# Performance work log

Measured on AMD Instinct MI355X. Metric: run time of the kernel, lower is better.

## Reference

```python
import jax, jax.numpy as jnp
import numpy as np

N_FILT = 80
FILT_DIM = 251
FS = 16000.0
MIN_FREQ = 50.0


def _kernel_gauss(amp, f1, f2, t):
    # Gaussian-windowed (Gabor-like) bandpass impulse response: band edges f1<f2 (Hz)
    fc = 0.5 * (f1 + f2)
    bw = f2 - f1
    return amp * jnp.exp(-2.0 * (jnp.pi * bw) ** 2 * t ** 2) * jnp.cos(2.0 * jnp.pi * fc * t)


def _norm_pm1(ir):
    # per-filter: scale to [-1,1] then zero-mean, matching the torch code
    mn = jnp.min(ir, axis=-1, keepdims=True)
    mx = jnp.max(ir, axis=-1, keepdims=True)
    ir = 2.0 * (ir - mn) / (mx - mn + 1e-6) - 1.0
    return ir - jnp.mean(ir, axis=-1, keepdims=True)


def _build_filters(norm_f1, norm_f2, norm_f3, norm_f4, amp1, amp2):
    N = FILT_DIM
    t = (jnp.arange(1, N + 1, dtype=jnp.float32) / FS)  # linspace(1,N,N)/fs
    mf = MIN_FREQ / FS
    f1 = jnp.clip(jnp.abs(norm_f1) + mf, 0.0, 0.5)
    f2 = jnp.clip(f1 + jnp.abs(norm_f2 - f1) + mf, 0.0, 0.5)
    f3 = jnp.clip(jnp.abs(norm_f3) + mf, 0.0, 0.5)
    f4 = jnp.clip(f3 + jnp.abs(norm_f4 - f3) + mf, 0.0, 0.5)
    a1 = jnp.abs(amp1)[:, None]
    a2 = jnp.abs(amp2)[:, None]
    ir1 = _norm_pm1(_kernel_gauss(a1, (f1 * FS)[:, None], (f2 * FS)[:, None], t[None, :]))
    ir2 = _norm_pm1(_kernel_gauss(a2, (f3 * FS)[:, None], (f4 * FS)[:, None], t[None, :]))
    pad = N // 2
    # cross-correlation of ir1 with ir2 (torch conv1d semantics), padding N//2 -> length N (N odd)
    def xcorr(a, b):
        return jnp.correlate(jnp.pad(a, (pad, pad)), b[::-1], mode='valid')[::-1] if False else jnp.convolve(jnp.pad(a, (pad, pad)), b[::-1], mode='valid')
    casc = jax.vmap(xcorr)(ir1, ir2)  # [N_filt, N]
    casc = _norm_pm1(casc)
    n = jnp.linspace(0.0, N, N)
    window = (0.54 - 0.46 * jnp.cos(2.0 * jnp.pi * n / N)).astype(jnp.float32)
    return casc * window[None, :]  # [N_filt, N]


def setup_inputs() -> dict:
    key = jax.random.key(0)
    ks = jax.random.split(key, 5)
    x = jax.random.normal(ks[0], (8, 1, 64000), dtype=jnp.float32)
    norm_f1 = jax.random.uniform(ks[1], (N_FILT,), dtype=jnp.float32) * 0.3
    norm_f2 = norm_f1 + jax.random.uniform(ks[2], (N_FILT,), dtype=jnp.float32) * 0.05
    norm_f3 = jax.random.uniform(ks[3], (N_FILT,), dtype=jnp.float32) * 0.3
    norm_f4 = norm_f3 + jax.random.uniform(ks[4], (N_FILT,), dtype=jnp.float32) * 0.05
    amp1 = jnp.ones((N_FILT,), dtype=jnp.float32)
    amp2 = jnp.ones((N_FILT,), dtype=jnp.float32)
    return {"x": x, "norm_f1": norm_f1, "norm_f2": norm_f2, "norm_f3": norm_f3,
            "norm_f4": norm_f4, "amp1": amp1, "amp2": amp2}


def reference(x, norm_f1, norm_f2, norm_f3, norm_f4, amp1, amp2):
    filters = _build_filters(norm_f1, norm_f2, norm_f3, norm_f4, amp1, amp2)
    w = filters[:, None, :]  # [O=N_filt, I=1, K]
    out = jax.lax.conv_general_dilated(
        x, w, window_strides=(1,), padding='VALID',
        dimension_numbers=('NCH', 'OIH', 'NCH'))
    return out  # [B, N_filt, T-K+1]
```

## Files before the change

kernel.cpp:

```cpp
#include <hip/hip_runtime.h>

#define FDIM   251
#define NFILT  80
#define KPAD   256
#define T_IN   64000
#define T_OUT  63750
#define NCHUNK 512
#define NXB    125
#define NFT    5
#define CPYLEN 392
#define XSTOT  (8 * CPYLEN)

typedef short bf16x8 __attribute__((ext_vector_type(8)));
typedef float f32x4  __attribute__((ext_vector_type(4)));

__device__ __forceinline__ unsigned short f2bf(float f) {
  unsigned int u = __float_as_uint(f);
  unsigned int r = (u + 0x7fffu + ((u >> 16) & 1u)) >> 16;
  return (unsigned short)r;
}
__device__ __forceinline__ unsigned int packbf(float a, float b) {
  return (unsigned int)f2bf(a) | ((unsigned int)f2bf(b) << 16);
}

__device__ __forceinline__ void norm_pm1_shared(float* a, float* scratch, int tid) {
  float v  = (tid < FDIM) ? a[tid] : 0.f;
  float mn = (tid < FDIM) ? v : 1e30f;
  float mx = (tid < FDIM) ? v : -1e30f;
  #pragma unroll
  for (int o = 32; o > 0; o >>= 1) {
    mn = fminf(mn, __shfl_down(mn, o));
    mx = fmaxf(mx, __shfl_down(mx, o));
  }
  const int wid = tid >> 6;
  if ((tid & 63) == 0) { scratch[wid] = mn; scratch[4 + wid] = mx; }
  __syncthreads();
  if (tid == 0) {
    scratch[0] = fminf(fminf(scratch[0], scratch[1]), fminf(scratch[2], scratch[3]));
    scratch[4] = fmaxf(fmaxf(scratch[4], scratch[5]), fmaxf(scratch[6], scratch[7]));
  }
  __syncthreads();
  const float gmn = scratch[0], gmx = scratch[4];
  const float nv = 2.f * (v - gmn) / (gmx - gmn + 1e-6f) - 1.f;
  __syncthreads();
  float s = (tid < FDIM) ? nv : 0.f;
  #pragma unroll
  for (int o = 32; o > 0; o >>= 1) s += __shfl_down(s, o);
  if ((tid & 63) == 0) scratch[wid] = s;
  __syncthreads();
  if (tid == 0) scratch[0] = (scratch[0] + scratch[1] + scratch[2] + scratch[3]) / 251.f;
  __syncthreads();
  const float mean = scratch[0];
  if (tid < FDIM) a[tid] = nv - mean;
  __syncthreads();
}

__global__ __launch_bounds__(256) void build_filters_kernel(
    const float* __restrict__ nf1, const float* __restrict__ nf2,
    const float* __restrict__ nf3, const float* __restrict__ nf4,
    const float* __restrict__ amp1, const float* __restrict__ amp2,
    unsigned short* __restrict__ Wbf) {
  __shared__ float ir1[FDIM], ir2[FDIM], casc[FDIM];
  __shared__ float scratch[8];
  const int f = blockIdx.x, tid = threadIdx.x;
  const float FS  = 16000.f;
  const float MF  = 50.f / 16000.f;
  const float PIF = 3.14159265358979323846f;
  const float TPI = 6.28318530717958647692f;

  const float f1 = fminf(fmaxf(fabsf(nf1[f]) + MF, 0.f), 0.5f);
  const float f2 = fminf(fmaxf(f1 + fabsf(nf2[f] - f1) + MF, 0.f), 0.5f);
  const float f3 = fminf(fmaxf(fabsf(nf3[f]) + MF, 0.f), 0.5f);
  const float f4 = fminf(fmaxf(f3 + fabsf(nf4[f] - f3) + MF, 0.f), 0.5f);
  const float a1 = fabsf(amp1[f]);
  const float a2 = fabsf(amp2[f]);

  if (tid < FDIM) {
    const float t = (float)(tid + 1) / FS;
    {
      const float fcs = 0.5f * (f1 + f2) * FS, bws = (f2 - f1) * FS;
      const float pb = PIF * bws;
      ir1[tid] = a1 * expf(-2.f * pb * pb * (t * t)) * cosf(TPI * fcs * t);
    }
    {
      const float fcs = 0.5f * (f3 + f4) * FS, bws = (f4 - f3) * FS;
      const float pb = PIF * bws;
      ir2[tid] = a2 * expf(-2.f * pb * pb * (t * t)) * cosf(TPI * fcs * t);
    }
  }
  __syncthreads();
  norm_pm1_shared(ir1, scratch, tid);
  norm_pm1_shared(ir2, scratch, tid);

  if (tid < FDIM) {
    const int i = tid;
    const int plo = (i - 125 > 0) ? (i - 125) : 0;
    const int phi = (i + 125 < 250) ? (i + 125) : 250;
    float s = 0.f;
    for (int p = plo; p <= phi; ++p) s += ir1[p] * ir2[p + 125 - i];
    casc[i] = s;
  }
  __syncthreads();
  norm_pm1_shared(casc, scratch, tid);

  if (tid < KPAD) {
    float v = 0.f;
    if (tid < FDIM) {
      const float win = 0.54f - 0.46f * cosf(TPI * ((float)tid / 250.f));
      v = casc[tid] * win;
    }
    Wbf[(size_t)f * KPAD + tid] = f2bf(v);
  }
}

__global__ __launch_bounds__(256, 4) void conv_mfma_kernel(
    const float* __restrict__ xin, const unsigned short* __restrict__ Wbf,
    float* __restrict__ outp) {
  __shared__ __align__(16) unsigned int xs[XSTOT];
  const int tid = threadIdx.x;
  const int n0  = blockIdx.x * NCHUNK;
  const int b   = blockIdx.y;
  const int l   = tid & 63, w = tid >> 6;
  const int m   = l & 15, h = l >> 4;

  const float* xg = xin + (size_t)b * T_IN;
  for (int i = tid; i < CPYLEN - 4; i += 256) {
    float e[10];
    #pragma unroll
    for (int q = 0; q < 10; ++q) {
      const int g = n0 + 2 * i + q;
      e[q] = (g < T_IN) ? xg[g] : 0.f;
    }
    #pragma unroll
    for (int j = 0; j < 8; ++j)
      xs[j * CPYLEN + i] = packbf(e[j], e[j + 1]);
  }
  __syncthreads();

  const unsigned int* psrc = xs + (m & 7) * CPYLEN;
  const int lane_q = h + (m >> 3);
  const int tw0 = w * 128;
  const short* Wp = (const short*)Wbf;

  #pragma unroll 1
  for (int ft = 0; ft < NFT; ++ft) {
    bf16x8 afr[8];
    #pragma unroll
    for (int c = 0; c < 8; ++c)
      afr[c] = *(const bf16x8*)(Wp + (ft * 16 + m) * KPAD + c * 32 + h * 8);

    const size_t rowh = ((size_t)b * NFILT + ft * 16 + 4 * h) * T_OUT;

    for (int jp = 0; jp < 4; ++jp) {
      const int qA = ((tw0 + jp * 32) >> 3) + lane_q;
      f32x4 accA = (f32x4){0.f, 0.f, 0.f, 0.f};
      f32x4 accB = (f32x4){0.f, 0.f, 0.f, 0.f};

      #pragma unroll
      for (int c = 0; c < 8; ++c) {
        const bf16x8 xa = *(const bf16x8*)(psrc + 4 * (qA + 4 * c));
        const bf16x8 xb = *(const bf16x8*)(psrc + 4 * (qA + 2 + 4 * c));
        accA = __builtin_amdgcn_mfma_f32_16x16x32_bf16(afr[c], xa, accA, 0, 0, 0);
        accB = __builtin_amdgcn_mfma_f32_16x16x32_bf16(afr[c], xb, accB, 0, 0, 0);
      }

      const int tgA = n0 + tw0 + jp * 32 + m;
      const int tgB = tgA + 16;
      #pragma unroll
      for (int r = 0; r < 4; ++r) {
        const size_t rb = rowh + (size_t)r * T_OUT;
        if (tgA < T_OUT) outp[rb + tgA] = accA[r];
        if (tgB < T_OUT) outp[rb + tgB] = accB[r];
      }
    }
  }
}

extern "C" void kernel_launch(void* const* d_in, const int* in_sizes, int n_in,
                              void* d_out, int out_size, void* d_ws, size_t ws_size,
                              hipStream_t stream) {
  const float* x    = (const float*)d_in[0];
  const float* nf1  = (const float*)d_in[1];
  const float* nf2  = (const float*)d_in[2];
  const float* nf3  = (const float*)d_in[3];
  const float* nf4  = (const float*)d_in[4];
  const float* amp1 = (const float*)d_in[5];
  const float* amp2 = (const float*)d_in[6];
  unsigned short* Wbf = (unsigned short*)d_ws;
  float* out = (float*)d_out;

  build_filters_kernel<<<NFILT, 256, 0, stream>>>(nf1, nf2, nf3, nf4, amp1, amp2, Wbf);

  dim3 grid(NXB, 8);
  conv_mfma_kernel<<<grid, 256, 0, stream>>>(x, Wbf, out);
}
```

Before: 69.05 us.

## Split conv into MFMA producer waves and store consumer waves via LDS double buffer

Doubles the block to 512 threads. Four waves compute MFMA tiles into a double-buffered LDS output staging area, and four other waves copy the previous filter tile to global memory with coalesced float2 stores. This overlaps compute with output writes and replaces the strided scattered per-lane stores with contiguous row writes. In exchange it uses about 66KB of extra LDS per block, which limits occupancy, and adds a block-wide barrier per stage.

```diff
diff --git a/kernel.cpp b/kernel.cpp
--- a/kernel.cpp
+++ b/kernel.cpp
@@ -10,6 +10,8 @@
 #define NFT    5
 #define CPYLEN 392
 #define XSTOT  (8 * CPYLEN)
+#define BUFSTR 514
+#define BUFSZ  (16 * BUFSTR)
 
 typedef short bf16x8 __attribute__((ext_vector_type(8)));
 typedef float f32x4  __attribute__((ext_vector_type(4)));
@@ -113,18 +115,19 @@
   }
 }
 
-__global__ __launch_bounds__(256, 4) void conv_mfma_kernel(
+__global__ __launch_bounds__(512, 4) void conv_mfma_kernel(
     const float* __restrict__ xin, const unsigned short* __restrict__ Wbf,
     float* __restrict__ outp) {
   __shared__ __align__(16) unsigned int xs[XSTOT];
+  __shared__ __align__(16) float obuf[2 * BUFSZ];
   const int tid = threadIdx.x;
   const int n0  = blockIdx.x * NCHUNK;
   const int b   = blockIdx.y;
-  const int l   = tid & 63, w = tid >> 6;
+  const int l   = tid & 63, wid = tid >> 6;
   const int m   = l & 15, h = l >> 4;
 
   const float* xg = xin + (size_t)b * T_IN;
-  for (int i = tid; i < CPYLEN - 4; i += 256) {
+  for (int i = tid; i < CPYLEN - 4; i += 512) {
     float e[10];
     #pragma unroll
     for (int q = 0; q < 10; ++q) {
@@ -139,40 +142,61 @@
 
   const unsigned int* psrc = xs + (m & 7) * CPYLEN;
   const int lane_q = h + (m >> 3);
+  const short* Wp = (const short*)Wbf;
+  const int w   = wid & 3;
   const int tw0 = w * 128;
-  const short* Wp = (const short*)Wbf;
+  const int wid2 = wid - 4;
 
   #pragma unroll 1
-  for (int ft = 0; ft < NFT; ++ft) {
-    bf16x8 afr[8];
-    #pragma unroll
-    for (int c = 0; c < 8; ++c)
-      afr[c] = *(const bf16x8*)(Wp + (ft * 16 + m) * KPAD + c * 32 + h * 8);
-
-    const size_t rowh = ((size_t)b * NFILT + ft * 16 + 4 * h) * T_OUT;
-
-    for (int jp = 0; jp < 4; ++jp) {
-      const int qA = ((tw0 + jp * 32) >> 3) + lane_q;
-      f32x4 accA = (f32x4){0.f, 0.f, 0.f, 0.f};
-      f32x4 accB = (f32x4){0.f, 0.f, 0.f, 0.f};
-
-      #pragma unroll
-      for (int c = 0; c < 8; ++c) {
-        const bf16x8 xa = *(const bf16x8*)(psrc + 4 * (qA + 4 * c));
-        const bf16x8 xb = *(const bf16x8*)(psrc + 4 * (qA + 2 + 4 * c));
-        accA = __builtin_amdgcn_mfma_f32_16x16x32_bf16(afr[c], xa, accA, 0, 0, 0);
-        accB = __builtin_amdgcn_mfma_f32_16x16x32_bf16(afr[c], xb, accB, 0, 0, 0);
+  for (int p = 0; p < NFT + 1; ++p) {
+    if (wid < 4) {
+      if (p < NFT) {
+        const int ft = p;
+        bf16x8 afr[8];
+        #pragma unroll
+        for (int c = 0; c < 8; ++c)
+          afr[c] = *(const bf16x8*)(Wp + (ft * 16 + m) * KPAD + c * 32 + h * 8);
+
+        float* buf = &obuf[(p & 1) * BUFSZ];
+        for (int jp = 0; jp < 4; ++jp) {
+          const int qA = ((tw0 + jp * 32) >> 3) + lane_q;
+          f32x4 accA = (f32x4){0.f, 0.f, 0.f, 0.f};
+          f32x4 accB = (f32x4){0.f, 0.f, 0.f, 0.f};
+          #pragma unroll
+          for (int c = 0; c < 8; ++c) {
+            const bf16x8 xa = *(const bf16x8*)(psrc + 4 * (qA + 4 * c));
+            const bf16x8 xb = *(const bf16x8*)(psrc + 4 * (qA + 2 + 4 * c));
+            accA = __builtin_amdgcn_mfma_f32_16x16x32_bf16(afr[c], xa, accA, 0, 0, 0);
+            accB = __builtin_amdgcn_mfma_f32_16x16x32_bf16(afr[c], xb, accB, 0, 0, 0);
+          }
+          const int tA = tw0 + jp * 32 + m;
+          #pragma unroll
+          for (int r = 0; r < 4; ++r) {
+            buf[(4 * h + r) * BUFSTR + tA]      = accA[r];
+            buf[(4 * h + r) * BUFSTR + tA + 16] = accB[r];
+          }
+        }
       }
-
-      const int tgA = n0 + tw0 + jp * 32 + m;
-      const int tgB = tgA + 16;
-      #pragma unroll
-      for (int r = 0; r < 4; ++r) {
-        const size_t rb = rowh + (size_t)r * T_OUT;
-        if (tgA < T_OUT) outp[rb + tgA] = accA[r];
-        if (tgB < T_OUT) outp[rb + tgB] = accB[r];
+    } else {
+      if (p >= 1) {
+        const int ft = p - 1;
+        const float* buf = &obuf[((p - 1) & 1) * BUFSZ];
+        #pragma unroll
+        for (int q = 0; q < 4; ++q) {
+          const int row = 4 * wid2 + q;
+          const size_t rb = ((size_t)b * NFILT + ft * 16 + row) * T_OUT + n0;
+          #pragma unroll
+          for (int seg = 0; seg < 4; ++seg) {
+            const int off = seg * 128 + 2 * l;
+            if (n0 + off < T_OUT) {
+              const float2 v = *(const float2*)&buf[row * BUFSTR + off];
+              *(float2*)&outp[rb + off] = v;
+            }
+          }
+        }
       }
     }
+    __syncthreads();
   }
 }
 
@@ -192,5 +216,5 @@
   build_filters_kernel<<<NFILT, 256, 0, stream>>>(nf1, nf2, nf3, nf4, amp1, amp2, Wbf);
 
   dim3 grid(NXB, 8);
-  conv_mfma_kernel<<<grid, 256, 0, stream>>>(x, Wbf, out);
-}
+  conv_mfma_kernel<<<grid, 512, 0, stream>>>(x, Wbf, out);
+}
```

Result: faster. 64.14 us (-7.1%).
